# Optimization experiments

Hardware: AMD Instinct MI355X
Metric: run time of the kernel (lower is better)

The kernel has to match this reference:

```python
import jax, jax.numpy as jnp
import numpy as np

N, E, F_IN, HID, HEADS = 10000, 160000, 70, 256, 4
NEG_SLOPE = 0.2


def setup_inputs() -> dict:
    key = jax.random.key(0)
    ks = jax.random.split(key, 12)
    p = lambda k, shape: jax.random.normal(k, shape, jnp.float32) * 0.05
    return dict(
        node_features=jax.random.normal(ks[0], (N, F_IN), jnp.float32),
        edge_index=jax.random.randint(ks[1], (2, E), 0, N),
        edge_attr=jax.random.normal(ks[2], (E, 4), jnp.float32),
        W1=p(ks[3], (F_IN, HEADS * HID)),
        att_src1=p(ks[4], (HEADS, HID)),
        att_dst1=p(ks[5], (HEADS, HID)),
        b1=jnp.zeros((HEADS * HID,), jnp.float32),
        W2=p(ks[6], (HEADS * HID, HID)),
        att_src2=p(ks[7], (1, HID)),
        att_dst2=p(ks[8], (1, HID)),
        b2=jnp.zeros((HID,), jnp.float32),
        Wv1=p(ks[9], (HID, 128)),
        bv1=jnp.zeros((128,), jnp.float32),
        Wv2=p(ks[10], (128, 1)),
        bv2=jnp.zeros((1,), jnp.float32),
    )


def _gat_layer(x, src, dst, W, a_src, a_dst, b, heads, ch, concat):
    """PyG GATConv (edge_dim=None, add_self_loops already applied to src/dst)."""
    n = x.shape[0]
    h = (x @ W).reshape(n, heads, ch)                      # [N,H,C]
    a_s = (h * a_src).sum(-1)                              # [N,H]
    a_d = (h * a_dst).sum(-1)                              # [N,H]
    e = jax.nn.leaky_relu(a_s[src] + a_d[dst], NEG_SLOPE)  # [E,H]
    # segment softmax over incoming edges of each destination node
    m = jax.ops.segment_max(e, dst, num_segments=n)        # [N,H]
    m = jnp.where(jnp.isfinite(m), m, 0.0)
    ex = jnp.exp(e - m[dst])
    denom = jax.ops.segment_sum(ex, dst, num_segments=n)[dst] + 1e-16
    alpha = ex / denom                                     # [E,H]
    out = jax.ops.segment_sum(h[src] * alpha[..., None], dst, num_segments=n)  # [N,H,C]
    out = out.reshape(n, heads * ch) if concat else out.mean(axis=1)
    return out + b


def reference(node_features, edge_index, edge_attr, W1, att_src1, att_dst1, b1,
              W2, att_src2, att_dst2, b2, Wv1, bv1, Wv2, bv2):
    # edge_attr is ignored: GATConv built without edge_dim has lin_edge=None.
    n = node_features.shape[0]
    loops = jnp.arange(n, dtype=edge_index.dtype)
    src = jnp.concatenate([edge_index[0], loops])
    dst = jnp.concatenate([edge_index[1], loops])
    x = jax.nn.relu(_gat_layer(node_features, src, dst, W1, att_src1, att_dst1, b1, HEADS, HID, True))
    x = jax.nn.relu(_gat_layer(x, src, dst, W2, att_src2, att_dst2, b2, 1, HID, False))
    pooled = x.mean(axis=0, keepdims=True)                 # [1,HID]
    hmid = jax.nn.gelu(pooled @ Wv1 + bv1, approximate=False)
    return hmid @ Wv2 + bv2                                # [1,1]
```

## Files before the change

kernel.cpp:

```cpp
#include <hip/hip_runtime.h>
#include <math.h>

#define NN   10000
#define NE   160000
#define NET  (NE + NN)
#define FIN  70
#define HIDC 256
#define NH   4
#define D1   1024
#define SLOPE 0.2f
#define KL1  96
#define NPB  32
#define BCAP 64

typedef float f32x4 __attribute__((ext_vector_type(4)));
typedef short bf16x8 __attribute__((ext_vector_type(8)));
typedef unsigned short u16x4 __attribute__((ext_vector_type(4)));

__device__ __forceinline__ unsigned short f32_to_bf16(float f) {
    unsigned int u = __float_as_uint(f);
    unsigned int r = u + 0x7fffu + ((u >> 16) & 1u);
    return (unsigned short)(r >> 16);
}
__device__ __forceinline__ float bf16_to_f32(unsigned short h) {
    return __uint_as_float(((unsigned int)h) << 16);
}
__device__ __forceinline__ float leaky(float e) { return (e > 0.f) ? e : SLOPE * e; }

__device__ __forceinline__ void cp16(const unsigned short* g, unsigned short* l) {
    __builtin_amdgcn_global_load_lds((const __attribute__((address_space(1))) unsigned int*)g,
                                     (__attribute__((address_space(3))) unsigned int*)l,
                                     16, 0, 0);
}

__global__ __launch_bounds__(256) void k_prep(const float* __restrict__ W2,
                                              unsigned short* __restrict__ W2t,
                                              const float* __restrict__ W1,
                                              unsigned short* __restrict__ W1t,
                                              const float* __restrict__ asrc,
                                              const float* __restrict__ adst,
                                              float* __restrict__ was,
                                              float* __restrict__ wad,
                                              const float* __restrict__ x,
                                              unsigned short* __restrict__ xb,
                                              const int* __restrict__ ei,
                                              int* __restrict__ cnt,
                                              int* __restrict__ ssrc) {
    __shared__ __align__(16) char smem[64 * 100 * 2];
    int b = blockIdx.x, t = threadIdx.x;
    if (b < 64) {
        unsigned short (*tl)[68] = (unsigned short (*)[68])smem;
        int kk0 = (b >> 2) * 64;
        int n0  = (b & 3) * 64;
        for (int i = t; i < 64 * 64; i += 256) {
            int nl = i & 63, kl = i >> 6;
            tl[nl][kl] = f32_to_bf16(W2[(size_t)(kk0 + kl) * HIDC + n0 + nl]);
        }
        __syncthreads();
        for (int i = t; i < 64 * 64; i += 256) {
            int kl = i & 63, nl = i >> 6;
            W2t[(size_t)(n0 + nl) * 1024 + kk0 + kl] = tl[nl][kl];
        }
    } else if (b < 80) {
        unsigned short (*tl)[97] = (unsigned short (*)[97])smem;
        int r0 = (b - 64) * 64;
        for (int i = t; i < 64 * 96; i += 256) {
            int rl = i & 63, kk = i >> 6;
            float w = (kk < FIN) ? W1[(size_t)kk * D1 + r0 + rl] : 0.f;
            tl[rl][kk] = f32_to_bf16(w);
        }
        __syncthreads();
        for (int i = t; i < 64 * 96; i += 256) {
            int kk = i % 96, rl = i / 96;
            W1t[(size_t)(r0 + rl) * KL1 + kk] = tl[rl][kk];
        }
    } else if (b < 80 + FIN) {
        int k = b - 80;
        float* rs = (float*)smem;
        float* rd = rs + 256;
#pragma unroll
        for (int h = 0; h < NH; h++) {
            float wv = W1[(size_t)k * D1 + h * 256 + t];
            rs[t] = wv * asrc[h * 256 + t];
            rd[t] = wv * adst[h * 256 + t];
            __syncthreads();
            for (int off = 128; off > 0; off >>= 1) {
                if (t < off) { rs[t] += rs[t + off]; rd[t] += rd[t + off]; }
                __syncthreads();
            }
            if (t == 0) { was[h * FIN + k] = rs[0]; wad[h * FIN + k] = rd[0]; }
            __syncthreads();
        }
    } else if (b < 80 + FIN + 40) {
        int b2 = b - 80 - FIN;
        size_t base = (size_t)b2 * 17500;
        for (int i = t; i < 17500; i += 256)
            xb[base + i] = f32_to_bf16(x[base + i]);
    } else {
        int e = (b - 80 - FIN - 40) * 256 + t;
        if (e < NET) {
            int src, dst;
            if (e < NE) { src = ei[e]; dst = ei[NE + e]; }
            else        { src = e - NE; dst = src; }
            int pos = atomicAdd(&cnt[dst], 1);
            if (pos < BCAP) ssrc[dst * BCAP + pos] = src;
        }
    }
}

__global__ __launch_bounds__(256) void k_att_x(const float* __restrict__ x,
                                               const float* __restrict__ was,
                                               const float* __restrict__ wad,
                                               float* __restrict__ asn,
                                               float* __restrict__ adn) {
    __shared__ float xs[64][71];
    int t = threadIdx.x;
    int n0 = blockIdx.x * 64;
    for (int i = t; i < 64 * FIN; i += 256) {
        int r = i / FIN, k = i % FIN;
        int n = n0 + r;
        xs[r][k] = (n < NN) ? x[(size_t)n * FIN + k] : 0.f;
    }
    __syncthreads();
    if (t >= 64) return;
    int n = n0 + t;
    if (n >= NN) return;
    float a[NH] = {}, d[NH] = {};
    for (int k = 0; k < FIN; k++) {
        float xv = xs[t][k];
#pragma unroll
        for (int h = 0; h < NH; h++) {
            a[h] += xv * was[h * FIN + k];
            d[h] += xv * wad[h * FIN + k];
        }
    }
#pragma unroll
    for (int h = 0; h < NH; h++) { asn[n * NH + h] = a[h]; adn[n * NH + h] = d[h]; }
}

__global__ __launch_bounds__(64) void k_sm_aggX(const int* __restrict__ cnt,
                                                const int* __restrict__ ssrc,
                                                const float* __restrict__ as,
                                                const float* __restrict__ ad,
                                                const unsigned short* __restrict__ xb,
                                                unsigned short* __restrict__ aggXhi) {
    int d = blockIdx.x, t = threadIdx.x;
    int n = cnt[d]; if (n > BCAP) n = BCAP;
    float4 adv = *(const float4*)&ad[d * NH];
    bool v0 = t < n;
    int s0 = 0;
    float e0[NH];
    if (v0) {
        s0 = ssrc[d * BCAP + t];
        float4 a4 = *(const float4*)&as[s0 * NH];
        e0[0] = leaky(a4.x + adv.x); e0[1] = leaky(a4.y + adv.y);
        e0[2] = leaky(a4.z + adv.z); e0[3] = leaky(a4.w + adv.w);
    } else { e0[0] = e0[1] = e0[2] = e0[3] = -1e30f; }
    float m[NH] = {e0[0], e0[1], e0[2], e0[3]};
#pragma unroll
    for (int h = 0; h < NH; h++)
        for (int off = 32; off > 0; off >>= 1)
            m[h] = fmaxf(m[h], __shfl_xor(m[h], off));
    float sum[NH];
#pragma unroll
    for (int h = 0; h < NH; h++) sum[h] = v0 ? expf(e0[h] - m[h]) : 0.f;
#pragma unroll
    for (int h = 0; h < NH; h++)
        for (int off = 32; off > 0; off >>= 1)
            sum[h] += __shfl_xor(sum[h], off);
    __shared__ float al4[64][4];
    __shared__ int   sid[64];
    if (v0) {
        sid[t] = s0;
#pragma unroll
        for (int h = 0; h < NH; h++) al4[t][h] = expf(e0[h] - m[h]) / (sum[h] + 1e-16f);
    }
    __syncthreads();
    float ac[NH][2] = {};
#pragma unroll 4
    for (int j = 0; j < n; j++) {
        int s = sid[j];
        float4 al = *(const float4*)al4[j];
        float xv0 = bf16_to_f32(xb[(size_t)s * FIN + t]);
        float xv1 = (t < FIN - 64) ? bf16_to_f32(xb[(size_t)s * FIN + 64 + t]) : 0.f;
        ac[0][0] += al.x * xv0; ac[0][1] += al.x * xv1;
        ac[1][0] += al.y * xv0; ac[1][1] += al.y * xv1;
        ac[2][0] += al.z * xv0; ac[2][1] += al.z * xv1;
        ac[3][0] += al.w * xv0; ac[3][1] += al.w * xv1;
    }
#pragma unroll
    for (int h = 0; h < NH; h++) {
        size_t base = ((size_t)d * NH + h) * KL1;
        aggXhi[base + t] = f32_to_bf16(ac[h][0]);
        if (t < 32) {
            float v1 = (t < FIN - 64) ? ac[h][1] : 0.f;
            aggXhi[base + 64 + t] = f32_to_bf16(v1);
        }
    }
}

__global__ __launch_bounds__(256) void k_gemm_l1(const unsigned short* __restrict__ aggXhi,
                                                 const unsigned short* __restrict__ W1t,
                                                 const float* __restrict__ b1,
                                                 unsigned short* __restrict__ x2hi) {
    __shared__ unsigned short As[128 * 96];
    __shared__ unsigned short Bs[128 * 96];
    int t = threadIdx.x;
    int n0 = blockIdx.x * 128;
    int cb = blockIdx.y * 128;
    int h  = blockIdx.z;
    int lane = t & 63, wave = t >> 6, quad = lane >> 4, l16 = lane & 15;
    int wr = (wave & 1) * 64, wc = (wave >> 1) * 64;
#pragma unroll
    for (int q = 0; q < 6; q++) {
        int g = q * 256 + t;
        int row = g / 12, gr = g % 12;
        int ra = n0 + row; if (ra >= NN) ra = NN - 1;
        cp16(aggXhi + ((size_t)ra * NH + h) * KL1 + gr * 8, As + g * 8);
        cp16(W1t + (size_t)(h * 256 + cb + row) * KL1 + gr * 8, Bs + g * 8);
    }
    __syncthreads();
    f32x4 acc[4][4] = {};
#pragma unroll
    for (int kc = 0; kc < 3; kc++) {
        bf16x8 af[4], bf[4];
#pragma unroll
        for (int i = 0; i < 4; i++) af[i] = *(const bf16x8*)&As[(wr + i * 16 + l16) * KL1 + kc * 32 + quad * 8];
#pragma unroll
        for (int j = 0; j < 4; j++) bf[j] = *(const bf16x8*)&Bs[(wc + j * 16 + l16) * KL1 + kc * 32 + quad * 8];
#pragma unroll
        for (int i = 0; i < 4; i++)
#pragma unroll
            for (int j = 0; j < 4; j++)
                acc[i][j] = __builtin_amdgcn_mfma_f32_16x16x32_bf16(af[i], bf[j], acc[i][j], 0, 0, 0);
    }
#pragma unroll
    for (int i = 0; i < 4; i++)
#pragma unroll
        for (int j = 0; j < 4; j++) {
            int colg = h * 256 + cb + wc + j * 16 + l16;
            float bb = b1[colg];
#pragma unroll
            for (int reg = 0; reg < 4; reg++) {
                int r = n0 + wr + i * 16 + quad * 4 + reg;
                if (r >= NN) continue;
                float v = fmaxf(acc[i][j][reg] + bb, 0.f);
                x2hi[(size_t)r * D1 + colg] = f32_to_bf16(v);
            }
        }
}

__global__ __launch_bounds__(256) void k_gemm2(const unsigned short* __restrict__ x2hi,
                                               const unsigned short* __restrict__ W2t,
                                               const float* __restrict__ asrc,
                                               const float* __restrict__ adst,
                                               unsigned short* __restrict__ h2bf,
                                               float* __restrict__ as2,
                                               float* __restrict__ ad2) {
    __shared__ unsigned short As[64 * 64];
    __shared__ unsigned short Bs[128 * 64];
    int t = threadIdx.x;
    int n0 = blockIdx.x * 64;
    int cb = blockIdx.y * 128;
    int lane = t & 63, wave = t >> 6, quad = lane >> 4, l16 = lane & 15;
    int wr = (wave & 1) * 32, wc = (wave >> 1) * 64;
    const unsigned short* ga[2];
    unsigned short* la[2];
#pragma unroll
    for (int q = 0; q < 2; q++) {
        int g = q * 256 + t;
        int row = g >> 3, gr = g & 7;
        int ra = n0 + row; if (ra >= NN) ra = NN - 1;
        ga[q] = x2hi + (size_t)ra * D1 + gr * 8;
        la[q] = As + g * 8;
    }
    const unsigned short* gb[4];
    unsigned short* lb[4];
#pragma unroll
    for (int q = 0; q < 4; q++) {
        int g = q * 256 + t;
        int col = g >> 3, gr = g & 7;
        gb[q] = W2t + (size_t)(cb + col) * 1024 + gr * 8;
        lb[q] = Bs + g * 8;
    }
    f32x4 acc[2][4] = {};
    for (int kc = 0; kc < 16; kc++) {
        cp16(ga[0] + kc * 64, la[0]);
        cp16(ga[1] + kc * 64, la[1]);
#pragma unroll
        for (int q = 0; q < 4; q++) cp16(gb[q] + kc * 64, lb[q]);
        __syncthreads();
#pragma unroll
        for (int ks = 0; ks < 2; ks++) {
            bf16x8 af[2], bf[4];
#pragma unroll
            for (int i = 0; i < 2; i++) af[i] = *(const bf16x8*)&As[(wr + i * 16 + l16) * 64 + ks * 32 + quad * 8];
#pragma unroll
            for (int j = 0; j < 4; j++) bf[j] = *(const bf16x8*)&Bs[(wc + j * 16 + l16) * 64 + ks * 32 + quad * 8];
#pragma unroll
            for (int i = 0; i < 2; i++)
#pragma unroll
                for (int j = 0; j < 4; j++)
                    acc[i][j] = __builtin_amdgcn_mfma_f32_16x16x32_bf16(af[i], bf[j], acc[i][j], 0, 0, 0);
        }
        __syncthreads();
    }
    float a2[4], d2[4];
#pragma unroll
    for (int j = 0; j < 4; j++) {
        int c = cb + wc + j * 16 + l16;
        a2[j] = asrc[c];
        d2[j] = adst[c];
    }
    float asp[2][4] = {}, adp[2][4] = {};
#pragma unroll
    for (int i = 0; i < 2; i++)
#pragma unroll
        for (int j = 0; j < 4; j++) {
            int c = cb + wc + j * 16 + l16;
#pragma unroll
            for (int reg = 0; reg < 4; reg++) {
                int r = n0 + wr + i * 16 + quad * 4 + reg;
                float v = acc[i][j][reg];
                if (r < NN) h2bf[(size_t)r * HIDC + c] = f32_to_bf16(v);
                asp[i][reg] += v * a2[j];
                adp[i][reg] += v * d2[j];
            }
        }
#pragma unroll
    for (int mask = 1; mask < 16; mask <<= 1)
#pragma unroll
        for (int i = 0; i < 2; i++)
#pragma unroll
            for (int reg = 0; reg < 4; reg++) {
                asp[i][reg] += __shfl_xor(asp[i][reg], mask);
                adp[i][reg] += __shfl_xor(adp[i][reg], mask);
            }
    if (l16 == 0) {
#pragma unroll
        for (int i = 0; i < 2; i++)
#pragma unroll
            for (int reg = 0; reg < 4; reg++) {
                int r = n0 + wr + i * 16 + quad * 4 + reg;
                if (r < NN) {
                    atomicAdd(&as2[r], asp[i][reg]);
                    atomicAdd(&ad2[r], adp[i][reg]);
                }
            }
    }
}

__global__ __launch_bounds__(256) void k_sm_aggr2(const int* __restrict__ cnt,
                                                  const int* __restrict__ ssrc,
                                                  const float* __restrict__ as,
                                                  const float* __restrict__ ad,
                                                  const unsigned short* __restrict__ h2bf,
                                                  const float* __restrict__ b,
                                                  float* __restrict__ pooled32) {
    int t = threadIdx.x, lane = t & 63, wave = t >> 6;
    int d = blockIdx.x * 4 + wave;
    int n = cnt[d]; if (n > BCAP) n = BCAP;
    float adv = ad[d];
    bool v0 = lane < n;
    int s0 = v0 ? ssrc[d * BCAP + lane] : 0;
    float e0 = v0 ? leaky(as[s0] + adv) : -1e30f;
    float m = e0;
    for (int off = 32; off > 0; off >>= 1) m = fmaxf(m, __shfl_xor(m, off));
    float ex = v0 ? expf(e0 - m) : 0.f;
    float sum = ex;
    for (int off = 32; off > 0; off >>= 1) sum += __shfl_xor(sum, off);
    float al0 = ex * (1.0f / (sum + 1e-16f));
    float a0 = 0.f, a1 = 0.f, a2 = 0.f, a3 = 0.f;
#pragma unroll 4
    for (int j = 0; j < n; j++) {
        float alj = __shfl(al0, j);
        int   sj  = __shfl(s0, j);
        u16x4 hv = *(const u16x4*)&h2bf[(size_t)sj * HIDC + lane * 4];
        a0 += alj * bf16_to_f32(hv[0]);
        a1 += alj * bf16_to_f32(hv[1]);
        a2 += alj * bf16_to_f32(hv[2]);
        a3 += alj * bf16_to_f32(hv[3]);
    }
    float4 bb = *(const float4*)&b[lane * 4];
    __shared__ float sacc[4][256];
    *(float4*)&sacc[wave][lane * 4] = make_float4(fmaxf(a0 + bb.x, 0.f),
                                                  fmaxf(a1 + bb.y, 0.f),
                                                  fmaxf(a2 + bb.z, 0.f),
                                                  fmaxf(a3 + bb.w, 0.f));
    __syncthreads();
    float s = sacc[0][t] + sacc[1][t] + sacc[2][t] + sacc[3][t];
    atomicAdd(&pooled32[(blockIdx.x & (NPB - 1)) * HIDC + t], s);
}

__global__ __launch_bounds__(128) void k_mlp(const float* __restrict__ pooled32,
                                             const float* __restrict__ Wv1,
                                             const float* __restrict__ bv1,
                                             const float* __restrict__ Wv2,
                                             const float* __restrict__ bv2,
                                             float* __restrict__ out) {
    int j = threadIdx.x;
    __shared__ float ps[256];
    for (int c = j; c < HIDC; c += 128) {
        float s = 0.f;
        for (int bkt = 0; bkt < NPB; bkt++) s += pooled32[bkt * HIDC + c];
        ps[c] = s;
    }
    __syncthreads();
    float s = bv1[j];
    const float invn = 1.0f / (float)NN;
    for (int c = 0; c < HIDC; c++)
        s += (ps[c] * invn) * Wv1[c * 128 + j];
    float g = 0.5f * s * (1.0f + erff(s * 0.70710678118654752f));
    float v = g * Wv2[j];
    __shared__ float red[128];
    red[j] = v;
    __syncthreads();
    for (int off = 64; off > 0; off >>= 1) {
        if (j < off) red[j] += red[j + off];
        __syncthreads();
    }
    if (j == 0) out[0] = red[0] + bv2[0];
}

extern "C" void kernel_launch(void* const* d_in, const int* in_sizes, int n_in,
                              void* d_out, int out_size, void* d_ws, size_t ws_size,
                              hipStream_t stream) {
    const float* x_in  = (const float*)d_in[0];
    const int*   ei    = (const int*)d_in[1];
    const float* W1    = (const float*)d_in[3];
    const float* asrc1 = (const float*)d_in[4];
    const float* adst1 = (const float*)d_in[5];
    const float* b1    = (const float*)d_in[6];
    const float* W2    = (const float*)d_in[7];
    const float* asrc2 = (const float*)d_in[8];
    const float* adst2 = (const float*)d_in[9];
    const float* b2    = (const float*)d_in[10];
    const float* Wv1   = (const float*)d_in[11];
    const float* bv1   = (const float*)d_in[12];
    const float* Wv2   = (const float*)d_in[13];
    const float* bv2   = (const float*)d_in[14];
    float* out = (float*)d_out;

    char* w = (char*)d_ws;
    auto alloc = [&](size_t bytes) { char* p = w; w += (bytes + 255) & ~(size_t)255; return p; };
    unsigned short* x2hi   = (unsigned short*)alloc(2ull * NN * D1);
    unsigned short* aggXhi = (unsigned short*)alloc(2ull * NN * NH * KL1);
    unsigned short* h2bf = (unsigned short*)alloc(2ull * NN * HIDC);
    unsigned short* xb   = (unsigned short*)alloc(2ull * NN * FIN);
    unsigned short* W2t  = (unsigned short*)alloc(2ull * 256 * 1024);
    unsigned short* W1t  = (unsigned short*)alloc(2ull * NH * 256 * KL1);
    float* as1    = (float*)alloc(sizeof(float) * NN * NH);
    float* ad1    = (float*)alloc(sizeof(float) * NN * NH);
    float* was1   = (float*)alloc(sizeof(float) * NH * FIN);
    float* wad1   = (float*)alloc(sizeof(float) * NH * FIN);
    int*   ssrc   = (int*)alloc(sizeof(int) * NN * BCAP);
    char*  zbase  = alloc(NN * 4 + NPB * HIDC * 4 + NN * 4 + NN * 4);
    int*   cnt      = (int*)zbase;
    float* pooled32 = (float*)(zbase + NN * 4);
    float* as2      = (float*)(zbase + NN * 4 + NPB * HIDC * 4);
    float* ad2      = (float*)(zbase + NN * 4 + NPB * HIDC * 4 + NN * 4);

    hipMemsetAsync(zbase, 0, NN * 4 + NPB * HIDC * 4 + NN * 4 + NN * 4, stream);

    k_prep<<<64 + 16 + FIN + 40 + 665, 256, 0, stream>>>(
        W2, W2t, W1, W1t, asrc1, adst1, was1, wad1, x_in, xb, ei, cnt, ssrc);
    k_att_x<<<157, 256, 0, stream>>>(x_in, was1, wad1, as1, ad1);

    k_sm_aggX<<<NN, 64, 0, stream>>>(cnt, ssrc, as1, ad1, xb, aggXhi);
    {
        dim3 g((NN + 127) / 128, 2, NH);
        k_gemm_l1<<<g, 256, 0, stream>>>(aggXhi, W1t, b1, x2hi);
    }

    {
        dim3 g((NN + 63) / 64, 2);
        k_gemm2<<<g, 256, 0, stream>>>(x2hi, W2t, asrc2, adst2, h2bf, as2, ad2);
    }
    k_sm_aggr2<<<NN / 4, 256, 0, stream>>>(cnt, ssrc, as2, ad2, h2bf, b2, pooled32);

    k_mlp<<<1, 128, 0, stream>>>(pooled32, Wv1, bv1, Wv2, bv2, out);
}
```

Before: 200.3 us.

## Fold attention-logit prep into k_prep and fuse MLP head into last aggregation block

Removes two kernel launches. k_att_x is merged into k_prep: each block recomputes the folded W1·att vectors with a wave-shuffle reduction instead of reading a precomputed table. k_mlp runs in the last-finishing block of k_sm_aggr2, found through a done counter after a threadfence. The x-to-bf16 conversion is also vectorised with float4 loads. In exchange, the W1·att work is duplicated across 157 blocks, and the fused head adds a serial tail to one block.

```diff
diff --git a/kernel.cpp b/kernel.cpp
--- a/kernel.cpp
+++ b/kernel.cpp
@@ -39,19 +39,19 @@
                                               unsigned short* __restrict__ W1t,
                                               const float* __restrict__ asrc,
                                               const float* __restrict__ adst,
-                                              float* __restrict__ was,
-                                              float* __restrict__ wad,
                                               const float* __restrict__ x,
                                               unsigned short* __restrict__ xb,
                                               const int* __restrict__ ei,
                                               int* __restrict__ cnt,
-                                              int* __restrict__ ssrc) {
-    __shared__ __align__(16) char smem[64 * 100 * 2];
+                                              int* __restrict__ ssrc,
+                                              float* __restrict__ asn,
+                                              float* __restrict__ adn) {
+    __shared__ __align__(16) char smem[20480];
     int b = blockIdx.x, t = threadIdx.x;
+    int lane = t & 63, wave = t >> 6;
     if (b < 64) {
         unsigned short (*tl)[68] = (unsigned short (*)[68])smem;
-        int kk0 = (b >> 2) * 64;
-        int n0  = (b & 3) * 64;
+        int kk0 = (b >> 2) * 64, n0 = (b & 3) * 64;
         for (int i = t; i < 64 * 64; i += 256) {
             int nl = i & 63, kl = i >> 6;
             tl[nl][kl] = f32_to_bf16(W2[(size_t)(kk0 + kl) * HIDC + n0 + nl]);
@@ -74,30 +74,17 @@
             int kk = i % 96, rl = i / 96;
             W1t[(size_t)(r0 + rl) * KL1 + kk] = tl[rl][kk];
         }
-    } else if (b < 80 + FIN) {
-        int k = b - 80;
-        float* rs = (float*)smem;
-        float* rd = rs + 256;
-#pragma unroll
-        for (int h = 0; h < NH; h++) {
-            float wv = W1[(size_t)k * D1 + h * 256 + t];
-            rs[t] = wv * asrc[h * 256 + t];
-            rd[t] = wv * adst[h * 256 + t];
-            __syncthreads();
-            for (int off = 128; off > 0; off >>= 1) {
-                if (t < off) { rs[t] += rs[t + off]; rd[t] += rd[t + off]; }
-                __syncthreads();
-            }
-            if (t == 0) { was[h * FIN + k] = rs[0]; wad[h * FIN + k] = rd[0]; }
-            __syncthreads();
-        }
-    } else if (b < 80 + FIN + 40) {
-        int b2 = b - 80 - FIN;
-        size_t base = (size_t)b2 * 17500;
-        for (int i = t; i < 17500; i += 256)
-            xb[base + i] = f32_to_bf16(x[base + i]);
-    } else {
-        int e = (b - 80 - FIN - 40) * 256 + t;
+    } else if (b < 120) {
+        size_t base = (size_t)(b - 80) * 17500;
+        for (int v = t; v < 4375; v += 256) {
+            float4 xv = *(const float4*)&x[base + v * 4];
+            u16x4 o;
+            o[0] = f32_to_bf16(xv.x); o[1] = f32_to_bf16(xv.y);
+            o[2] = f32_to_bf16(xv.z); o[3] = f32_to_bf16(xv.w);
+            *(u16x4*)&xb[base + v * 4] = o;
+        }
+    } else if (b < 785) {
+        int e = (b - 120) * 256 + t;
         if (e < NET) {
             int src, dst;
             if (e < NE) { src = ei[e]; dst = ei[NE + e]; }
@@ -105,37 +92,55 @@
             int pos = atomicAdd(&cnt[dst], 1);
             if (pos < BCAP) ssrc[dst * BCAP + pos] = src;
         }
-    }
-}
-
-__global__ __launch_bounds__(256) void k_att_x(const float* __restrict__ x,
-                                               const float* __restrict__ was,
-                                               const float* __restrict__ wad,
-                                               float* __restrict__ asn,
-                                               float* __restrict__ adn) {
-    __shared__ float xs[64][71];
-    int t = threadIdx.x;
-    int n0 = blockIdx.x * 64;
-    for (int i = t; i < 64 * FIN; i += 256) {
-        int r = i / FIN, k = i % FIN;
-        int n = n0 + r;
-        xs[r][k] = (n < NN) ? x[(size_t)n * FIN + k] : 0.f;
-    }
-    __syncthreads();
-    if (t >= 64) return;
-    int n = n0 + t;
-    if (n >= NN) return;
-    float a[NH] = {}, d[NH] = {};
-    for (int k = 0; k < FIN; k++) {
-        float xv = xs[t][k];
-#pragma unroll
-        for (int h = 0; h < NH; h++) {
-            a[h] += xv * was[h * FIN + k];
-            d[h] += xv * wad[h * FIN + k];
-        }
-    }
-#pragma unroll
-    for (int h = 0; h < NH; h++) { asn[n * NH + h] = a[h]; adn[n * NH + h] = d[h]; }
+    } else {
+        int n0 = (b - 785) * 64;
+        float (*xs)[71] = (float (*)[71])smem;
+        float* lws = (float*)(smem + 64 * 71 * 4);
+        float* lwd = lws + NH * FIN;
+        for (int i = t; i < 64 * FIN; i += 256) {
+            int r = i / FIN, k = i % FIN;
+            int n = n0 + r;
+            xs[r][k] = (n < NN) ? x[(size_t)n * FIN + k] : 0.f;
+        }
+        float ar[16], dr[16];
+#pragma unroll
+        for (int q = 0; q < 4; q++) {
+            float4 av = *(const float4*)&asrc[lane * 16 + q * 4];
+            float4 dv = *(const float4*)&adst[lane * 16 + q * 4];
+            ar[q*4+0]=av.x; ar[q*4+1]=av.y; ar[q*4+2]=av.z; ar[q*4+3]=av.w;
+            dr[q*4+0]=dv.x; dr[q*4+1]=dv.y; dr[q*4+2]=dv.z; dr[q*4+3]=dv.w;
+        }
+        for (int k = wave; k < FIN; k += 4) {
+            const float* row = W1 + (size_t)k * D1 + lane * 16;
+            float s = 0.f, dd = 0.f;
+#pragma unroll
+            for (int q = 0; q < 4; q++) {
+                float4 wv = *(const float4*)(row + q * 4);
+                s  += wv.x*ar[q*4] + wv.y*ar[q*4+1] + wv.z*ar[q*4+2] + wv.w*ar[q*4+3];
+                dd += wv.x*dr[q*4] + wv.y*dr[q*4+1] + wv.z*dr[q*4+2] + wv.w*dr[q*4+3];
+            }
+#pragma unroll
+            for (int off = 1; off < 16; off <<= 1) { s += __shfl_xor(s, off); dd += __shfl_xor(dd, off); }
+            if ((lane & 15) == 0) { int h = lane >> 4; lws[h * FIN + k] = s; lwd[h * FIN + k] = dd; }
+        }
+        __syncthreads();
+        if (t < 64) {
+            int n = n0 + t;
+            if (n < NN) {
+                float a[NH] = {}, d2[NH] = {};
+                for (int k = 0; k < FIN; k++) {
+                    float xv = xs[t][k];
+#pragma unroll
+                    for (int h = 0; h < NH; h++) {
+                        a[h]  += xv * lws[h * FIN + k];
+                        d2[h] += xv * lwd[h * FIN + k];
+                    }
+                }
+#pragma unroll
+                for (int h = 0; h < NH; h++) { asn[n*NH+h] = a[h]; adn[n*NH+h] = d2[h]; }
+            }
+        }
+    }
 }
 
 __global__ __launch_bounds__(64) void k_sm_aggX(const int* __restrict__ cnt,
@@ -356,7 +361,13 @@
                                                   const float* __restrict__ ad,
                                                   const unsigned short* __restrict__ h2bf,
                                                   const float* __restrict__ b,
-                                                  float* __restrict__ pooled32) {
+                                                  float* __restrict__ pooled32,
+                                                  int* __restrict__ donecnt,
+                                                  const float* __restrict__ Wv1,
+                                                  const float* __restrict__ bv1,
+                                                  const float* __restrict__ Wv2,
+                                                  const float* __restrict__ bv2,
+                                                  float* __restrict__ out) {
     int t = threadIdx.x, lane = t & 63, wave = t >> 6;
     int d = blockIdx.x * 4 + wave;
     int n = cnt[d]; if (n > BCAP) n = BCAP;
@@ -370,56 +381,55 @@
     float sum = ex;
     for (int off = 32; off > 0; off >>= 1) sum += __shfl_xor(sum, off);
     float al0 = ex * (1.0f / (sum + 1e-16f));
-    float a0 = 0.f, a1 = 0.f, a2 = 0.f, a3 = 0.f;
+    float a0 = 0.f, a1 = 0.f, a2v = 0.f, a3 = 0.f;
 #pragma unroll 4
     for (int j = 0; j < n; j++) {
         float alj = __shfl(al0, j);
         int   sj  = __shfl(s0, j);
         u16x4 hv = *(const u16x4*)&h2bf[(size_t)sj * HIDC + lane * 4];
-        a0 += alj * bf16_to_f32(hv[0]);
-        a1 += alj * bf16_to_f32(hv[1]);
-        a2 += alj * bf16_to_f32(hv[2]);
-        a3 += alj * bf16_to_f32(hv[3]);
+        a0  += alj * bf16_to_f32(hv[0]);
+        a1  += alj * bf16_to_f32(hv[1]);
+        a2v += alj * bf16_to_f32(hv[2]);
+        a3  += alj * bf16_to_f32(hv[3]);
     }
     float4 bb = *(const float4*)&b[lane * 4];
-    __shared__ float sacc[4][256];
-    *(float4*)&sacc[wave][lane * 4] = make_float4(fmaxf(a0 + bb.x, 0.f),
-                                                  fmaxf(a1 + bb.y, 0.f),
-                                                  fmaxf(a2 + bb.z, 0.f),
-                                                  fmaxf(a3 + bb.w, 0.f));
-    __syncthreads();
-    float s = sacc[0][t] + sacc[1][t] + sacc[2][t] + sacc[3][t];
+    __shared__ float sacc[4 * 256];
+    *(float4*)&sacc[wave * 256 + lane * 4] = make_float4(fmaxf(a0 + bb.x, 0.f),
+                                                         fmaxf(a1 + bb.y, 0.f),
+                                                         fmaxf(a2v + bb.z, 0.f),
+                                                         fmaxf(a3 + bb.w, 0.f));
+    __syncthreads();
+    float s = sacc[t] + sacc[256 + t] + sacc[512 + t] + sacc[768 + t];
     atomicAdd(&pooled32[(blockIdx.x & (NPB - 1)) * HIDC + t], s);
-}
-
-__global__ __launch_bounds__(128) void k_mlp(const float* __restrict__ pooled32,
-                                             const float* __restrict__ Wv1,
-                                             const float* __restrict__ bv1,
-                                             const float* __restrict__ Wv2,
-                                             const float* __restrict__ bv2,
-                                             float* __restrict__ out) {
-    int j = threadIdx.x;
-    __shared__ float ps[256];
-    for (int c = j; c < HIDC; c += 128) {
-        float s = 0.f;
-        for (int bkt = 0; bkt < NPB; bkt++) s += pooled32[bkt * HIDC + c];
-        ps[c] = s;
-    }
-    __syncthreads();
-    float s = bv1[j];
-    const float invn = 1.0f / (float)NN;
-    for (int c = 0; c < HIDC; c++)
-        s += (ps[c] * invn) * Wv1[c * 128 + j];
-    float g = 0.5f * s * (1.0f + erff(s * 0.70710678118654752f));
-    float v = g * Wv2[j];
-    __shared__ float red[128];
-    red[j] = v;
+
+    __threadfence();
+    __syncthreads();
+    __shared__ int lastblk;
+    if (t == 0) lastblk = (atomicAdd(donecnt, 1) == (NN / 4) - 1);
+    __syncthreads();
+    if (!lastblk) return;
+
+    float* ps  = sacc;
+    float* red = sacc + 256;
+    float s0sum = 0.f;
+    for (int bkt = 0; bkt < NPB; bkt++)
+        s0sum += atomicAdd(&pooled32[bkt * HIDC + t], 0.0f);
+    ps[t] = s0sum;
+    __syncthreads();
+    if (t < 128) {
+        float sv = bv1[t];
+        const float invn = 1.0f / (float)NN;
+        for (int c = 0; c < HIDC; c++)
+            sv += (ps[c] * invn) * Wv1[c * 128 + t];
+        float g = 0.5f * sv * (1.0f + erff(sv * 0.70710678118654752f));
+        red[t] = g * Wv2[t];
+    }
     __syncthreads();
     for (int off = 64; off > 0; off >>= 1) {
-        if (j < off) red[j] += red[j + off];
-        __syncthreads();
-    }
-    if (j == 0) out[0] = red[0] + bv2[0];
+        if (t < off) red[t] += red[t + off];
+        __syncthreads();
+    }
+    if (t == 0) out[0] = red[0] + bv2[0];
 }
 
 extern "C" void kernel_launch(void* const* d_in, const int* in_sizes, int n_in,
@@ -451,20 +461,19 @@
     unsigned short* W1t  = (unsigned short*)alloc(2ull * NH * 256 * KL1);
     float* as1    = (float*)alloc(sizeof(float) * NN * NH);
     float* ad1    = (float*)alloc(sizeof(float) * NN * NH);
-    float* was1   = (float*)alloc(sizeof(float) * NH * FIN);
-    float* wad1   = (float*)alloc(sizeof(float) * NH * FIN);
     int*   ssrc   = (int*)alloc(sizeof(int) * NN * BCAP);
-    char*  zbase  = alloc(NN * 4 + NPB * HIDC * 4 + NN * 4 + NN * 4);
+    size_t zbytes = (size_t)NN * 4 + NPB * HIDC * 4 + NN * 4 + NN * 4 + 4;
+    char*  zbase  = alloc(zbytes);
     int*   cnt      = (int*)zbase;
     float* pooled32 = (float*)(zbase + NN * 4);
     float* as2      = (float*)(zbase + NN * 4 + NPB * HIDC * 4);
     float* ad2      = (float*)(zbase + NN * 4 + NPB * HIDC * 4 + NN * 4);
-
-    hipMemsetAsync(zbase, 0, NN * 4 + NPB * HIDC * 4 + NN * 4 + NN * 4, stream);
-
-    k_prep<<<64 + 16 + FIN + 40 + 665, 256, 0, stream>>>(
-        W2, W2t, W1, W1t, asrc1, adst1, was1, wad1, x_in, xb, ei, cnt, ssrc);
-    k_att_x<<<157, 256, 0, stream>>>(x_in, was1, wad1, as1, ad1);
+    int*   donecnt  = (int*)(zbase + NN * 4 + NPB * HIDC * 4 + NN * 4 + NN * 4);
+
+    hipMemsetAsync(zbase, 0, zbytes, stream);
+
+    k_prep<<<64 + 16 + 40 + 665 + 157, 256, 0, stream>>>(
+        W2, W2t, W1, W1t, asrc1, adst1, x_in, xb, ei, cnt, ssrc, as1, ad1);
 
     k_sm_aggX<<<NN, 64, 0, stream>>>(cnt, ssrc, as1, ad1, xb, aggXhi);
     {
@@ -476,7 +485,7 @@
         dim3 g((NN + 63) / 64, 2);
         k_gemm2<<<g, 256, 0, stream>>>(x2hi, W2t, asrc2, adst2, h2bf, as2, ad2);
     }
-    k_sm_aggr2<<<NN / 4, 256, 0, stream>>>(cnt, ssrc, as2, ad2, h2bf, b2, pooled32);
-
-    k_mlp<<<1, 128, 0, stream>>>(pooled32, Wv1, bv1, Wv2, bv2, out);
-}
+
+    k_sm_aggr2<<<NN / 4, 256, 0, stream>>>(cnt, ssrc, as2, ad2, h2bf, b2, pooled32,
+                                           donecnt, Wv1, bv1, Wv2, bv2, out);
+}
```

Result: slower. 354.3 us (+76.9%).
